# Kernel tuning notes

Measured on AMD Instinct MI355X. Metric: run time of the kernel, lower is better.

## Reference

```python
import jax, jax.numpy as jnp
import numpy as np

N = 100000   # nodes
E = 1600000  # edges (before self-loops)
IN = 128     # m (input feature dim)
H = 64       # hidden
L = 8        # layers
OUT = 40     # m_y


def setup_inputs() -> dict:
    key = jax.random.key(0)
    ks = jax.random.split(key, 6)
    x = jax.random.normal(ks[0], (N, IN), dtype=jnp.float32)
    edge_index = jax.random.randint(ks[1], (2, E), 0, N, dtype=jnp.int64)
    W0 = jax.random.normal(ks[2], (IN, H), dtype=jnp.float32) / np.float32(np.sqrt(IN))
    Ws = jax.random.normal(ks[3], (L - 1, H, H), dtype=jnp.float32) / np.float32(np.sqrt(H))
    bs = jnp.zeros((L, H), dtype=jnp.float32)
    lin_w = jax.random.normal(ks[4], (L * H, OUT), dtype=jnp.float32) / np.float32(np.sqrt(L * H))
    lin_b = jnp.zeros((OUT,), dtype=jnp.float32)
    return dict(x=x, W0=W0, Ws=Ws, bs=bs, lin_w=lin_w, lin_b=lin_b, edge_index=edge_index)


def reference(x, W0, Ws, bs, lin_w, lin_b, edge_index):
    # GCNConv (PyG): add self-loops, symmetric normalization D^-1/2 A D^-1/2.
    loop = jnp.arange(N, dtype=edge_index.dtype)
    src = jnp.concatenate([edge_index[0], loop])  # message sources
    dst = jnp.concatenate([edge_index[1], loop])  # aggregation targets
    deg = jax.ops.segment_sum(jnp.ones_like(dst, dtype=x.dtype), dst, num_segments=N)
    dis = jnp.where(deg > 0, jax.lax.rsqrt(deg), jnp.zeros_like(deg))
    norm = dis[src] * dis[dst]  # [E+N]

    def gcn_conv(h, W, b):
        h = h @ W                           # linear transform first (PyG order)
        msg = h[src] * norm[:, None]        # gather + edge normalization
        return jax.ops.segment_sum(msg, dst, num_segments=N) + b

    # dropout(p=0.5) is identity in eval mode (training=False)
    outs = []
    h = x
    for l in range(L):  # fixed small layer count
        W = W0 if l == 0 else Ws[l - 1]
        h = jax.nn.relu(gcn_conv(h, W, bs[l]))
        outs.append(h)
    jk = jnp.concatenate(outs, axis=-1)     # JumpingKnowledge 'cat': [N, L*H]
    return jk @ lin_w + lin_b
```

## Files before the change

kernel.cpp:

```cpp
#include <hip/hip_runtime.h>
#include <hip/hip_bf16.h>
#include <hip/hip_fp16.h>

#define N_NODES 100000
#define N_EDGES 1600000
#define HID     64
#define LAYERS  8
#define OUT_DIM 40
#define SCAN_NB 98
#define ZROW    N_NODES
#define NBUK    196
#define BUK_CAP 12000
#define S1_EPB  2048
#define AGG_N   32
#define AGG_CAP 1024

typedef __attribute__((ext_vector_type(8))) short short8;
typedef __attribute__((ext_vector_type(8))) _Float16 half8;
typedef __attribute__((ext_vector_type(4))) float float4v;
typedef __attribute__((ext_vector_type(4))) unsigned int uint4v;

__device__ inline float ldext(const void* p, bool f32, size_t i) {
    return f32 ? ((const float*)p)[i]
               : __bfloat162float(((const __hip_bfloat16*)p)[i]);
}
__device__ inline int load_edge(const void* raw, bool is64, long long idx) {
    return is64 ? (int)((const long long*)raw)[idx] : ((const int*)raw)[idx];
}
__device__ inline unsigned pack_bf16x2(float lo, float hi) {
    union { __hip_bfloat16 b; unsigned short u; } a, b;
    a.b = __float2bfloat16(lo);
    b.b = __float2bfloat16(hi);
    return ((unsigned)b.u << 16) | a.u;
}
__device__ inline unsigned short bf16bits(float v) {
    union { __hip_bfloat16 b; unsigned short u; } a;
    a.b = __float2bfloat16(v);
    return a.u;
}
__device__ inline unsigned short f16bits(float v) {
    union { __half h; unsigned short u; } a;
    a.h = __float2half_rn(v);
    return a.u;
}
__device__ inline __half2 u2h2(unsigned u) {
    union { unsigned u; __half2 h; } x; x.u = u; return x.h;
}
__device__ inline unsigned h22u(__half2 h) {
    union { unsigned u; __half2 h; } x; x.h = h; return x.u;
}

template <int CTRL>
__device__ inline unsigned dppu(unsigned v) {
    return (unsigned)__builtin_amdgcn_update_dpp((int)v, (int)v, CTRL, 0xF, 0xF, false);
}

__device__ inline uint4v gload16(const __half* base, unsigned voff) {
    uint4v d;
    asm volatile("global_load_dwordx4 %0, %1, %2"
                 : "=v"(d)
                 : "v"(voff), "s"((unsigned long long)base));
    return d;
}
#define WAITV(N) do { asm volatile("s_waitcnt vmcnt(" #N ")" ::: "memory"); \
                      __builtin_amdgcn_sched_barrier(0); } while (0)

__global__ void detect_kernel(const void* x, const void* ei, int* flags, int* gcur) {
    int t = threadIdx.x;
    for (int i = t; i < NBUK; i += 64) gcur[i] = 0;
    float v = fabsf(__bfloat162float(((const __hip_bfloat16*)x)[t]));
    bool inband = (v >= 0.00390625f && v <= 16.0f);
    unsigned long long m = __ballot(inband);
    if (t == 0) {
        flags[0] = (__popcll(m) < 48) ? 1 : 0;
        const int* e32 = (const int*)ei;
        flags[1] = ((e32[1] | e32[3] | e32[5] | e32[7]) == 0) ? 1 : 0;
    }
}

__global__ __launch_bounds__(256) void pack_params_kernel(const void* bs, const void* lin_w,
                                                          const void* W0, const void* Ws,
                                                          const int* __restrict__ flags,
                                                          float* __restrict__ bsf,
                                                          unsigned short* __restrict__ wpack) {
    bool f32 = flags[0] != 0;
    int gid = blockIdx.x * 256 + threadIdx.x;
    int stride = gridDim.x * 256;
    for (int idx = gid; idx < LAYERS * HID; idx += stride) bsf[idx] = ldext(bs, f32, idx);
    for (int idx = gid; idx < 8192; idx += stride) {
        int j = idx & 7, lane = (idx >> 3) & 63, rest = idx >> 9;
        int ks = rest & 3, ct = rest >> 2;
        int quad = lane >> 4, m = lane & 15;
        wpack[idx] = bf16bits(ldext(W0, f32, (size_t)(ks * 32 + quad * 8 + j) * 64 + ct * 16 + m));
    }
    for (int idx = gid; idx < 7 * 4096; idx += stride) {
        int l = idx >> 12, r = idx & 4095;
        int j = r & 7, lane = (r >> 3) & 63, rest = r >> 9;
        int ks = rest & 1, ct = rest >> 1;
        int quad = lane >> 4, m = lane & 15;
        wpack[8192 + idx] = f16bits(
            ldext(Ws, f32, (size_t)l * 4096 + (size_t)(ks * 32 + quad * 8 + j) * 64 + ct * 16 + m));
    }
    for (int idx = gid; idx < LAYERS * 3072; idx += stride) {
        int l = idx / 3072, r = idx % 3072;
        int j = r & 7, lane = (r >> 3) & 63, rest = r >> 9;
        int ks = rest & 1, ct = rest >> 1;
        int quad = lane >> 4, m = lane & 15;
        int col = ct * 16 + m;
        int k = l * 64 + ks * 32 + quad * 8 + j;
        wpack[36864 + idx] = (col < OUT_DIM)
            ? f16bits(ldext(lin_w, f32, (size_t)k * OUT_DIM + col)) : (unsigned short)0;
    }
}

__global__ __launch_bounds__(256) void bucket1_kernel(const void* ei_raw, const int* __restrict__ flags,
                                                      int* __restrict__ gcur, int* __restrict__ fifo) {
    __shared__ int lhist[NBUK];
    __shared__ int lbase[NBUK];
    bool is64 = flags[1] != 0;
    int t = threadIdx.x;
    for (int i = t; i < NBUK; i += 256) lhist[i] = 0;
    __syncthreads();
    int e0 = blockIdx.x * S1_EPB;
    int rec[8], bk[8], loff[8];
#pragma unroll
    for (int j = 0; j < 8; j++) {
        int e = e0 + j * 256 + t;
        bk[j] = -1;
        if (e < N_EDGES) {
            int s = load_edge(ei_raw, is64, e);
            int d = load_edge(ei_raw, is64, (long long)N_EDGES + e);
            int b = d >> 9;
            bk[j] = b;
            rec[j] = ((d & 511) << 17) | s;
            loff[j] = atomicAdd(&lhist[b], 1);
        }
    }
    __syncthreads();
    for (int i = t; i < NBUK; i += 256)
        lbase[i] = (lhist[i] > 0) ? atomicAdd(&gcur[i], lhist[i]) : 0;
    __syncthreads();
#pragma unroll
    for (int j = 0; j < 8; j++) {
        if (bk[j] >= 0) {
            int idx = lbase[bk[j]] + loff[j];
            if (idx < BUK_CAP) fifo[bk[j] * BUK_CAP + idx] = rec[j];
        }
    }
}

__global__ __launch_bounds__(256) void deg_fifo_kernel(const int* __restrict__ gcur,
                                                       const int* __restrict__ fifo,
                                                       int* __restrict__ deg,
                                                       float* __restrict__ dis) {
    __shared__ int ldeg[512];
    int b = blockIdx.x, t = threadIdx.x;
    ldeg[t] = 0;
    ldeg[t + 256] = 0;
    __syncthreads();
    int cnt = min(gcur[b], BUK_CAP);
    for (int i = t; i < cnt; i += 256)
        atomicAdd(&ldeg[fifo[b * BUK_CAP + i] >> 17], 1);
    __syncthreads();
    int n0 = b * 512 + t;
    if (n0 < N_NODES) {
        int d = ldeg[t];
        deg[n0] = d;
        dis[n0] = rsqrtf((float)(d + 1));
    }
    if (n0 + 256 < N_NODES) {
        int d = ldeg[t + 256];
        deg[n0 + 256] = d;
        dis[n0 + 256] = rsqrtf((float)(d + 1));
    }
}

__global__ __launch_bounds__(256) void scan1_kernel(const int* __restrict__ deg, int* __restrict__ row,
                                                    int* __restrict__ bsums) {
    __shared__ int sd[256];
    int t = threadIdx.x;
    int base = blockIdx.x * 1024 + t * 4;
    int v[4];
#pragma unroll
    for (int j = 0; j < 4; j++) {
        int idx = base + j;
        v[j] = (idx < N_NODES) ? deg[idx] : 0;
    }
    int s4 = v[0] + v[1] + v[2] + v[3];
    sd[t] = s4;
    __syncthreads();
    for (int off = 1; off < 256; off <<= 1) {
        int x = (t >= off) ? sd[t - off] : 0;
        __syncthreads();
        sd[t] += x;
        __syncthreads();
    }
    int run = sd[t] - s4;
#pragma unroll
    for (int j = 0; j < 4; j++) {
        int idx = base + j;
        if (idx < N_NODES) row[idx] = run;
        run += v[j];
    }
    if (t == 255) bsums[blockIdx.x] = sd[255];
}

__global__ void scan2_kernel(int* bsums) {
    __shared__ int sd[128];
    int t = threadIdx.x;
    int v = (t < SCAN_NB) ? bsums[t] : 0;
    sd[t] = v;
    __syncthreads();
    for (int off = 1; off < 128; off <<= 1) {
        int x = (t >= off) ? sd[t - off] : 0;
        __syncthreads();
        sd[t] += x;
        __syncthreads();
    }
    if (t < SCAN_NB) bsums[t] = sd[t] - v;
}

__global__ __launch_bounds__(256) void scan3_kernel(int* __restrict__ row, const int* __restrict__ bsums) {
    int i = blockIdx.x * 256 + threadIdx.x;
    if (i < N_NODES) row[i] += bsums[i >> 10];
    if (i == 0) row[N_NODES] = N_EDGES;
}

__global__ __launch_bounds__(256) void bucket2_kernel(const int* __restrict__ gcur,
                                                      const int* __restrict__ fifo,
                                                      const int* __restrict__ row,
                                                      int* __restrict__ csr_src) {
    __shared__ int lcur[512];
    int b = blockIdx.x, t = threadIdx.x;
    int n0 = b * 512 + t;
    lcur[t] = row[min(n0, N_NODES)];
    lcur[t + 256] = row[min(n0 + 256, N_NODES)];
    __syncthreads();
    int cnt = min(gcur[b], BUK_CAP);
    for (int i = t; i < cnt; i += 256) {
        int r = fifo[b * BUK_CAP + i];
        int pos = atomicAdd(&lcur[r >> 17], 1);
        csr_src[pos] = r & 0x1FFFF;
    }
}

template <int KS, int JK, bool ABF16>
__global__ __launch_bounds__(256) void mm_mfma_kernel(const void* __restrict__ h0,
                                                      const void* __restrict__ h1,
                                                      const int* __restrict__ flags,
                                                      const unsigned short* __restrict__ wW,
                                                      const unsigned short* __restrict__ wJ,
                                                      const float* __restrict__ dis,
                                                      __half* __restrict__ t0,
                                                      float* __restrict__ out_acc) {
    constexpr int K = KS * 32;
    int wave = threadIdx.x >> 6, lane = threadIdx.x & 63;
    int quad = lane >> 4, m = lane & 15;
    int nb = blockIdx.x * 64 + wave * 16;
    int ra = nb + m;
    if (ra > N_NODES - 1) ra = N_NODES - 1;
    short8 a[KS];
    if constexpr (ABF16) {
        if (flags[0]) {
            const float* xr = (const float*)h1 + (size_t)ra * K + quad * 8;
#pragma unroll
            for (int ks = 0; ks < KS; ks++) {
                float4 f0 = *(const float4*)(xr + ks * 32);
                float4 f1 = *(const float4*)(xr + ks * 32 + 4);
                short8 v;
                v[0] = (short)bf16bits(f0.x); v[1] = (short)bf16bits(f0.y);
                v[2] = (short)bf16bits(f0.z); v[3] = (short)bf16bits(f0.w);
                v[4] = (short)bf16bits(f1.x); v[5] = (short)bf16bits(f1.y);
                v[6] = (short)bf16bits(f1.z); v[7] = (short)bf16bits(f1.w);
                a[ks] = v;
            }
        } else {
            const short* hrow = (const short*)h0 + (size_t)ra * K + quad * 8;
#pragma unroll
            for (int ks = 0; ks < KS; ks++) a[ks] = *(const short8*)(hrow + ks * 32);
        }
    } else {
        const short* hrow = (const short*)h0 + (size_t)ra * K + quad * 8;
#pragma unroll
        for (int ks = 0; ks < KS; ks++) a[ks] = *(const short8*)(hrow + ks * 32);
    }
    float dr[4];
#pragma unroll
    for (int r = 0; r < 4; r++) {
        int rw = nb + quad * 4 + r;
        dr[r] = (rw < N_NODES) ? dis[rw] : 0.f;
    }
#pragma unroll
    for (int ct = 0; ct < 4; ct++) {
        float4v acc = (float4v){0.f, 0.f, 0.f, 0.f};
#pragma unroll
        for (int ks = 0; ks < KS; ks++) {
            short8 b = *(const short8*)(wW + ((ct * KS + ks) * 64 + lane) * 8);
            if constexpr (ABF16)
                acc = __builtin_amdgcn_mfma_f32_16x16x32_bf16(a[ks], b, acc, 0, 0, 0);
            else
                acc = __builtin_amdgcn_mfma_f32_16x16x32_f16(
                    __builtin_bit_cast(half8, a[ks]), __builtin_bit_cast(half8, b), acc, 0, 0, 0);
        }
#pragma unroll
        for (int r = 0; r < 4; r++) {
            t0[(size_t)(nb + quad * 4 + r) * 64 + ct * 16 + m] =
                __float2half(acc[r] * dr[r]);
        }
    }
    if (JK) {
#pragma unroll
        for (int ct = 0; ct < 3; ct++) {
            float4v j = (float4v){0.f, 0.f, 0.f, 0.f};
#pragma unroll
            for (int ks = 0; ks < KS; ks++) {
                short8 b = *(const short8*)(wJ + ((ct * KS + ks) * 64 + lane) * 8);
                if constexpr (ABF16)
                    j = __builtin_amdgcn_mfma_f32_16x16x32_bf16(a[ks], b, j, 0, 0, 0);
                else
                    j = __builtin_amdgcn_mfma_f32_16x16x32_f16(
                        __builtin_bit_cast(half8, a[ks]), __builtin_bit_cast(half8, b), j, 0, 0, 0);
            }
            int col = ct * 16 + m;
            if (col < OUT_DIM) {
#pragma unroll
                for (int r = 0; r < 4; r++) {
                    int rw = nb + quad * 4 + r;
                    if (rw < N_NODES) {
                        size_t o = (size_t)rw * OUT_DIM + col;
                        if (JK == 1) out_acc[o] = j[r];
                        else out_acc[o] += j[r];
                    }
                }
            }
        }
    }
}

__global__ __launch_bounds__(256, 6) void agg_kernel(const __half* __restrict__ t0,
                                                     const int* __restrict__ row,
                                                     const int* __restrict__ csr_src,
                                                     const float* __restrict__ bsf,
                                                     __half* __restrict__ h) {
    __shared__ int lrow[AGG_N + 1];
    __shared__ __align__(16) int lcsr[AGG_CAP + 32];
    int t = threadIdx.x;
    int nb = blockIdx.x * AGG_N;

    for (int i = t; i <= AGG_N; i += 256) {
        int n = nb + i;
        lrow[i] = row[n > N_NODES ? N_NODES : n];
    }
    __syncthreads();
    int rs0 = lrow[0];
    int cnt_raw = lrow[AGG_N] - rs0;
    int cnt = min(cnt_raw, AGG_CAP);

    int wave = t >> 6, lane = t & 63;
    for (int c = wave; c * 256 < cnt; c += 4) {
        const int* gsrc = csr_src + rs0 + c * 256 + lane * 4;
        __builtin_amdgcn_global_load_lds(
            (const __attribute__((address_space(1))) unsigned int*)gsrc,
            (__attribute__((address_space(3))) unsigned int*)&lcsr[4 + c * 256],
            16, 0, 0);
    }
    asm volatile("s_waitcnt vmcnt(0)" ::: "memory");
    __syncthreads();

    int g = lane >> 3, p = lane & 7;
    unsigned po = (unsigned)(p << 4);
    const __half2 h2zero = __floats2half2_rn(0.f, 0.f);

    if (cnt_raw <= AGG_CAP) {
        uint4v Av0, Av1, Av2; int Ars, Are;
        uint4v Bv0, Bv1, Bv2; int Brs, Bre;
        uint4v Cv0, Cv1, Cv2; int Crs, Cre;

#define AGG_ISSUE(P, v0, v1, v2, rs_, re_)                                      \
        do {                                                                    \
            int nl_ = wave * 8 + (P);                                           \
            int node_ = nb + nl_;                                               \
            bool valid_ = node_ < N_NODES;                                      \
            rs_ = valid_ ? lrow[nl_] : 0;                                       \
            re_ = valid_ ? lrow[nl_ + 1] : 0;                                   \
            int b_ = max(rs_ - rs0, 0) + g;                                     \
            int se0_ = lcsr[b_ + 3];                          \
            int se1_ = lcsr[b_ + 11];                         \
            int se2_ = lcsr[b_ + 19];                         \
            se0_ = (g == 0) ? (valid_ ? node_ : ZROW)                           \
                            : ((rs_ + g - 1 < re_) ? se0_ : ZROW);              \
            se1_ = (rs_ + g + 7  < re_) ? se1_ : ZROW;                          \
            se2_ = (rs_ + g + 15 < re_) ? se2_ : ZROW;                          \
            v0 = gload16(t0, ((unsigned)se0_ << 7) | po);                       \
            v1 = gload16(t0, ((unsigned)se1_ << 7) | po);                       \
            v2 = gload16(t0, ((unsigned)se2_ << 7) | po);                       \
        } while (0)

#define AGG_CONSUME(P, v0, v1, v2, rs_, re_)                                    \
        do {                                                                    \
            int nl_ = wave * 8 + (P);                                           \
            int node_ = nb + nl_;                                               \
            bool valid_ = node_ < N_NODES;                                      \
            __half2 a0_ = __hadd2(__hadd2(u2h2(v0[0]), u2h2(v1[0])), u2h2(v2[0])); \
            __half2 a1_ = __hadd2(__hadd2(u2h2(v0[1]), u2h2(v1[1])), u2h2(v2[1])); \
            __half2 a2_ = __hadd2(__hadd2(u2h2(v0[2]), u2h2(v1[2])), u2h2(v2[2])); \
            __half2 a3_ = __hadd2(__hadd2(u2h2(v0[3]), u2h2(v1[3])), u2h2(v2[3])); \
            if (__builtin_expect(__any(re_ - rs_ > 23), 0)) {                   \
                for (int q_ = rs_ + 23 + g; q_ < re_; q_ += 8) {                \
                    int se_ = lcsr[4 + q_ - rs0];                               \
                    uint4 v_ = *(const uint4*)(t0 + (size_t)se_ * 64 + p * 8);  \
                    a0_ = __hadd2(a0_, u2h2(v_.x));                             \
                    a1_ = __hadd2(a1_, u2h2(v_.y));                             \
                    a2_ = __hadd2(a2_, u2h2(v_.z));                             \
                    a3_ = __hadd2(a3_, u2h2(v_.w));                             \
                }                                                               \
            }                                                                   \
             \
            a0_ = __hadd2(a0_, u2h2(dppu<0x128>(h22u(a0_))));                   \
            a1_ = __hadd2(a1_, u2h2(dppu<0x128>(h22u(a1_))));                   \
            a2_ = __hadd2(a2_, u2h2(dppu<0x128>(h22u(a2_))));                   \
            a3_ = __hadd2(a3_, u2h2(dppu<0x128>(h22u(a3_))));                   \
            a0_ = __hadd2(a0_, u2h2(__shfl_xor(h22u(a0_), 16)));                \
            a1_ = __hadd2(a1_, u2h2(__shfl_xor(h22u(a1_), 16)));                \
            a2_ = __hadd2(a2_, u2h2(__shfl_xor(h22u(a2_), 16)));                \
            a3_ = __hadd2(a3_, u2h2(__shfl_xor(h22u(a3_), 16)));                \
            a0_ = __hadd2(a0_, u2h2(__shfl_xor(h22u(a0_), 32)));                \
            a1_ = __hadd2(a1_, u2h2(__shfl_xor(h22u(a1_), 32)));                \
            a2_ = __hadd2(a2_, u2h2(__shfl_xor(h22u(a2_), 32)));                \
            a3_ = __hadd2(a3_, u2h2(__shfl_xor(h22u(a3_), 32)));                \
            if (valid_ && g == 0) {                                             \
                float di_ = rsqrtf((float)(re_ - rs_ + 1));                     \
                const float* bb_ = bsf + p * 8;                                 \
                float f_[8];                                                    \
                f_[0] = __low2float(a0_); f_[1] = __high2float(a0_);            \
                f_[2] = __low2float(a1_); f_[3] = __high2float(a1_);            \
                f_[4] = __low2float(a2_); f_[5] = __high2float(a2_);            \
                f_[6] = __low2float(a3_); f_[7] = __high2float(a3_);            \
                _Pragma("unroll")                                               \
                for (int j_ = 0; j_ < 8; j_++)                                  \
                    f_[j_] = fmaxf(di_ * f_[j_] + bb_[j_], 0.f);                \
                uint4 pv_;                                                      \
                pv_.x = h22u(__floats2half2_rn(f_[0], f_[1]));                  \
                pv_.y = h22u(__floats2half2_rn(f_[2], f_[3]));                  \
                pv_.z = h22u(__floats2half2_rn(f_[4], f_[5]));                  \
                pv_.w = h22u(__floats2half2_rn(f_[6], f_[7]));                  \
                *(uint4*)(h + (size_t)node_ * 64 + p * 8) = pv_;                \
            }                                                                   \
        } while (0)

        AGG_ISSUE(0, Av0, Av1, Av2, Ars, Are);
        AGG_ISSUE(1, Bv0, Bv1, Bv2, Brs, Bre);
        AGG_ISSUE(2, Cv0, Cv1, Cv2, Crs, Cre);
        WAITV(6); AGG_CONSUME(0, Av0, Av1, Av2, Ars, Are);
        AGG_ISSUE(3, Av0, Av1, Av2, Ars, Are);
        WAITV(6); AGG_CONSUME(1, Bv0, Bv1, Bv2, Brs, Bre);
        AGG_ISSUE(4, Bv0, Bv1, Bv2, Brs, Bre);
        WAITV(6); AGG_CONSUME(2, Cv0, Cv1, Cv2, Crs, Cre);
        AGG_ISSUE(5, Cv0, Cv1, Cv2, Crs, Cre);
        WAITV(6); AGG_CONSUME(3, Av0, Av1, Av2, Ars, Are);
        AGG_ISSUE(6, Av0, Av1, Av2, Ars, Are);
        WAITV(6); AGG_CONSUME(4, Bv0, Bv1, Bv2, Brs, Bre);
        AGG_ISSUE(7, Bv0, Bv1, Bv2, Brs, Bre);
        WAITV(6); AGG_CONSUME(5, Cv0, Cv1, Cv2, Crs, Cre);
        WAITV(3); AGG_CONSUME(6, Av0, Av1, Av2, Ars, Are);
        WAITV(0); AGG_CONSUME(7, Bv0, Bv1, Bv2, Brs, Bre);
#undef AGG_ISSUE
#undef AGG_CONSUME
    } else {
        for (int pass = 0; pass < 8; pass++) {
            int nl = wave * 8 + pass;
            int node = nb + nl;
            bool valid = node < N_NODES;
            int rs = valid ? lrow[nl] : 0;
            int re = valid ? lrow[nl + 1] : 0;
            __half2 a2[4];
#pragma unroll
            for (int r = 0; r < 4; r++) a2[r] = h2zero;
            if (valid && g == 0) {
                uint4 v = *(const uint4*)(t0 + (size_t)node * 64 + p * 8);
                a2[0] = __hadd2(a2[0], u2h2(v.x));
                a2[1] = __hadd2(a2[1], u2h2(v.y));
                a2[2] = __hadd2(a2[2], u2h2(v.z));
                a2[3] = __hadd2(a2[3], u2h2(v.w));
            }
            for (int e = rs + g; e < re; e += 8) {
                int idx = e - rs0;
                int se = (idx < AGG_CAP) ? lcsr[4 + idx] : csr_src[e];
                uint4 v = *(const uint4*)(t0 + (size_t)se * 64 + p * 8);
                a2[0] = __hadd2(a2[0], u2h2(v.x));
                a2[1] = __hadd2(a2[1], u2h2(v.y));
                a2[2] = __hadd2(a2[2], u2h2(v.z));
                a2[3] = __hadd2(a2[3], u2h2(v.w));
            }
#pragma unroll
            for (int st = 8; st <= 32; st <<= 1) {
#pragma unroll
                for (int r = 0; r < 4; r++)
                    a2[r] = __hadd2(a2[r], u2h2(__shfl_xor(h22u(a2[r]), st)));
            }
            if (valid && g == 0) {
                float di = rsqrtf((float)(re - rs + 1));
                const float* bb = bsf + p * 8;
                float a[8];
#pragma unroll
                for (int r = 0; r < 4; r++) {
                    a[2 * r]     = __low2float(a2[r]);
                    a[2 * r + 1] = __high2float(a2[r]);
                }
#pragma unroll
                for (int j = 0; j < 8; j++) a[j] = fmaxf(di * a[j] + bb[j], 0.f);
                uint4 pv;
                pv.x = h22u(__floats2half2_rn(a[0], a[1]));
                pv.y = h22u(__floats2half2_rn(a[2], a[3]));
                pv.z = h22u(__floats2half2_rn(a[4], a[5]));
                pv.w = h22u(__floats2half2_rn(a[6], a[7]));
                *(uint4*)(h + (size_t)node * 64 + p * 8) = pv;
            }
        }
    }
}

__global__ __launch_bounds__(256) void jk_final_kernel(const __half* __restrict__ h,
                                                       const unsigned short* __restrict__ wJ,
                                                       const float* __restrict__ out_acc,
                                                       const void* __restrict__ lin_b,
                                                       const int* __restrict__ flags,
                                                       void* __restrict__ d_out) {
    bool f32 = flags[0] != 0;
    int wave = threadIdx.x >> 6, lane = threadIdx.x & 63;
    int quad = lane >> 4, m = lane & 15;
    int nb = blockIdx.x * 64 + wave * 16;
    int ra = nb + m;
    if (ra > N_NODES - 1) ra = N_NODES - 1;
    const short* hrow = (const short*)(h + (size_t)ra * 64) + quad * 8;
    short8 a0 = *(const short8*)(hrow);
    short8 a1 = *(const short8*)(hrow + 32);
#pragma unroll
    for (int ct = 0; ct < 3; ct++) {
        float4v j = (float4v){0.f, 0.f, 0.f, 0.f};
        short8 b0 = *(const short8*)(wJ + ((ct * 2 + 0) * 64 + lane) * 8);
        short8 b1 = *(const short8*)(wJ + ((ct * 2 + 1) * 64 + lane) * 8);
        j = __builtin_amdgcn_mfma_f32_16x16x32_f16(
            __builtin_bit_cast(half8, a0), __builtin_bit_cast(half8, b0), j, 0, 0, 0);
        j = __builtin_amdgcn_mfma_f32_16x16x32_f16(
            __builtin_bit_cast(half8, a1), __builtin_bit_cast(half8, b1), j, 0, 0, 0);
        int col = ct * 16 + m;
        if (col < OUT_DIM) {
            float lb = ldext(lin_b, f32, col);
#pragma unroll
            for (int r = 0; r < 4; r++) {
                int rw = nb + quad * 4 + r;
                if (rw < N_NODES) {
                    float v = out_acc[(size_t)rw * OUT_DIM + col] + j[r] + lb;
                    if (f32) ((float*)d_out)[(size_t)rw * OUT_DIM + col] = v;
                    else ((__hip_bfloat16*)d_out)[(size_t)rw * OUT_DIM + col] = __float2bfloat16(v);
                }
            }
        }
    }
}

extern "C" void kernel_launch(void* const* d_in, const int* in_sizes, int n_in,
                              void* d_out, int out_size, void* d_ws, size_t ws_size,
                              hipStream_t stream) {
    const void* x     = d_in[0];
    const void* W0    = d_in[1];
    const void* Ws    = d_in[2];
    const void* bs    = d_in[3];
    const void* lin_w = d_in[4];
    const void* lin_b = d_in[5];
    const void* ei    = d_in[6];

    size_t off = 0;
    auto alloc = [&](size_t bytes) -> void* {
        void* p = (char*)d_ws + off;
        off += (bytes + 511) & ~(size_t)511;
        return p;
    };
    int*   flags   = (int*)alloc(512);
    float* dis     = (float*)alloc((size_t)(N_NODES + 64) * 4);
    int*   deg     = (int*)alloc((size_t)N_NODES * 4);
    int*   row     = (int*)alloc((size_t)(N_NODES + 1) * 4);
    int*   bsums   = (int*)alloc(128 * 4);
    int*   gcur    = (int*)alloc((size_t)NBUK * 4);
    int*   fifo    = (int*)alloc((size_t)NBUK * BUK_CAP * 4);
    int*   csr_src = (int*)alloc((size_t)N_EDGES * 4);
    __half* t0  = (__half*)alloc((size_t)(N_NODES + 32) * HID * 2);
    __half* h   = (__half*)alloc((size_t)(N_NODES + 32) * HID * 2);
    float* out_acc = (float*)alloc((size_t)N_NODES * OUT_DIM * 4);
    float* bsf     = (float*)alloc((size_t)LAYERS * HID * 4);
    unsigned short* wpack = (unsigned short*)alloc((size_t)61440 * 2);

    const int nblkN  = (N_NODES + 255) / 256;
    const int nblkS1 = (N_EDGES + S1_EPB - 1) / S1_EPB;
    const int nblkMM = (N_NODES + 63) / 64;
    const int nblkAG = (N_NODES + AGG_N - 1) / AGG_N;

    detect_kernel<<<1, 64, 0, stream>>>(x, ei, flags, gcur);
    pack_params_kernel<<<80, 256, 0, stream>>>(bs, lin_w, W0, Ws, flags, bsf, wpack);
    bucket1_kernel<<<nblkS1, 256, 0, stream>>>(ei, flags, gcur, fifo);
    deg_fifo_kernel<<<NBUK, 256, 0, stream>>>(gcur, fifo, deg, dis);
    scan1_kernel<<<SCAN_NB, 256, 0, stream>>>(deg, row, bsums);
    scan2_kernel<<<1, 128, 0, stream>>>(bsums);
    scan3_kernel<<<nblkN, 256, 0, stream>>>(row, bsums);
    bucket2_kernel<<<NBUK, 256, 0, stream>>>(gcur, fifo, row, csr_src);

    const unsigned short* wJ0 = wpack + 36864;
    for (int l = 0; l < LAYERS; l++) {
        if (l == 0) {
            mm_mfma_kernel<4, 0, true><<<nblkMM, 256, 0, stream>>>(
                x, x, flags, wpack, nullptr, dis, t0, nullptr);
        } else if (l == 1) {
            mm_mfma_kernel<2, 1, false><<<nblkMM, 256, 0, stream>>>(
                h, h, flags, wpack + 8192, wJ0, dis, t0, out_acc);
        } else {
            mm_mfma_kernel<2, 2, false><<<nblkMM, 256, 0, stream>>>(
                h, h, flags, wpack + 8192 + (size_t)(l - 1) * 4096,
                wJ0 + (size_t)(l - 1) * 3072, dis, t0, out_acc);
        }
        agg_kernel<<<nblkAG, 256, 0, stream>>>(t0, row, csr_src,
                                               bsf + (size_t)l * HID, h);
    }
    jk_final_kernel<<<nblkMM, 256, 0, stream>>>(h, wJ0 + (size_t)7 * 3072, out_acc,
                                                lin_b, flags, d_out);
}
```

Before: 512.1 us.

## Fuse GCN aggregation with next layer's matmul and JK projection per block

Each layer's aggregation kernel now keeps its 64 output rows in shared memory and immediately runs the next layer's weight transform and JK output projection with MFMA. Half of the waves do the hidden transform while the other half do the JK accumulation. t0 ping-pongs between two buffers, so the separate matmul pass and the h round-trip through global memory go away. The block grows to 512 threads with a larger edge cache, which may reduce occupancy and makes the heavy MFMA work uneven across waves.

Result: faster. 493.3 us, median of 2 (-3.7%).

```diff
diff --git a/kernel.cpp b/kernel.cpp
--- a/kernel.cpp
+++ b/kernel.cpp
@@ -12,8 +12,9 @@
 #define NBUK    196
 #define BUK_CAP 12000
 #define S1_EPB  2048
-#define AGG_N   32
-#define AGG_CAP 1024
+#define FU_N    64
+#define FU_CAP  2048
+#define HB_S    72
 
 typedef __attribute__((ext_vector_type(8))) short short8;
 typedef __attribute__((ext_vector_type(8))) _Float16 half8;
@@ -26,12 +27,6 @@
 }
 __device__ inline int load_edge(const void* raw, bool is64, long long idx) {
     return is64 ? (int)((const long long*)raw)[idx] : ((const int*)raw)[idx];
-}
-__device__ inline unsigned pack_bf16x2(float lo, float hi) {
-    union { __hip_bfloat16 b; unsigned short u; } a, b;
-    a.b = __float2bfloat16(lo);
-    b.b = __float2bfloat16(hi);
-    return ((unsigned)b.u << 16) | a.u;
 }
 __device__ inline unsigned short bf16bits(float v) {
     union { __hip_bfloat16 b; unsigned short u; } a;
@@ -244,43 +239,33 @@
     }
 }
 
-template <int KS, int JK, bool ABF16>
-__global__ __launch_bounds__(256) void mm_mfma_kernel(const void* __restrict__ h0,
-                                                      const void* __restrict__ h1,
-                                                      const int* __restrict__ flags,
-                                                      const unsigned short* __restrict__ wW,
-                                                      const unsigned short* __restrict__ wJ,
-                                                      const float* __restrict__ dis,
-                                                      __half* __restrict__ t0,
-                                                      float* __restrict__ out_acc) {
-    constexpr int K = KS * 32;
+__global__ __launch_bounds__(256) void mm0_kernel(const void* __restrict__ x,
+                                                  const int* __restrict__ flags,
+                                                  const unsigned short* __restrict__ wW,
+                                                  const float* __restrict__ dis,
+                                                  __half* __restrict__ t0) {
+    constexpr int KS = 4, K = 128;
     int wave = threadIdx.x >> 6, lane = threadIdx.x & 63;
     int quad = lane >> 4, m = lane & 15;
     int nb = blockIdx.x * 64 + wave * 16;
     int ra = nb + m;
     if (ra > N_NODES - 1) ra = N_NODES - 1;
     short8 a[KS];
-    if constexpr (ABF16) {
-        if (flags[0]) {
-            const float* xr = (const float*)h1 + (size_t)ra * K + quad * 8;
-#pragma unroll
-            for (int ks = 0; ks < KS; ks++) {
-                float4 f0 = *(const float4*)(xr + ks * 32);
-                float4 f1 = *(const float4*)(xr + ks * 32 + 4);
-                short8 v;
-                v[0] = (short)bf16bits(f0.x); v[1] = (short)bf16bits(f0.y);
-                v[2] = (short)bf16bits(f0.z); v[3] = (short)bf16bits(f0.w);
-                v[4] = (short)bf16bits(f1.x); v[5] = (short)bf16bits(f1.y);
-                v[6] = (short)bf16bits(f1.z); v[7] = (short)bf16bits(f1.w);
-                a[ks] = v;
-            }
-        } else {
-            const short* hrow = (const short*)h0 + (size_t)ra * K + quad * 8;
-#pragma unroll
-            for (int ks = 0; ks < KS; ks++) a[ks] = *(const short8*)(hrow + ks * 32);
+    if (flags[0]) {
+        const float* xr = (const float*)x + (size_t)ra * K + quad * 8;
+#pragma unroll
+        for (int ks = 0; ks < KS; ks++) {
+            float4 f0 = *(const float4*)(xr + ks * 32);
+            float4 f1 = *(const float4*)(xr + ks * 32 + 4);
+            short8 v;
+            v[0] = (short)bf16bits(f0.x); v[1] = (short)bf16bits(f0.y);
+            v[2] = (short)bf16bits(f0.z); v[3] = (short)bf16bits(f0.w);
+            v[4] = (short)bf16bits(f1.x); v[5] = (short)bf16bits(f1.y);
+            v[6] = (short)bf16bits(f1.z); v[7] = (short)bf16bits(f1.w);
+            a[ks] = v;
         }
     } else {
-        const short* hrow = (const short*)h0 + (size_t)ra * K + quad * 8;
+        const short* hrow = (const short*)x + (size_t)ra * K + quad * 8;
 #pragma unroll
         for (int ks = 0; ks < KS; ks++) a[ks] = *(const short8*)(hrow + ks * 32);
     }
@@ -296,11 +281,7 @@
 #pragma unroll
         for (int ks = 0; ks < KS; ks++) {
             short8 b = *(const short8*)(wW + ((ct * KS + ks) * 64 + lane) * 8);
-            if constexpr (ABF16)
-                acc = __builtin_amdgcn_mfma_f32_16x16x32_bf16(a[ks], b, acc, 0, 0, 0);
-            else
-                acc = __builtin_amdgcn_mfma_f32_16x16x32_f16(
-                    __builtin_bit_cast(half8, a[ks]), __builtin_bit_cast(half8, b), acc, 0, 0, 0);
+            acc = __builtin_amdgcn_mfma_f32_16x16x32_bf16(a[ks], b, acc, 0, 0, 0);
         }
 #pragma unroll
         for (int r = 0; r < 4; r++) {
@@ -308,56 +289,37 @@
                 __float2half(acc[r] * dr[r]);
         }
     }
-    if (JK) {
-#pragma unroll
-        for (int ct = 0; ct < 3; ct++) {
-            float4v j = (float4v){0.f, 0.f, 0.f, 0.f};
-#pragma unroll
-            for (int ks = 0; ks < KS; ks++) {
-                short8 b = *(const short8*)(wJ + ((ct * KS + ks) * 64 + lane) * 8);
-                if constexpr (ABF16)
-                    j = __builtin_amdgcn_mfma_f32_16x16x32_bf16(a[ks], b, j, 0, 0, 0);
-                else
-                    j = __builtin_amdgcn_mfma_f32_16x16x32_f16(
-                        __builtin_bit_cast(half8, a[ks]), __builtin_bit_cast(half8, b), j, 0, 0, 0);
-            }
-            int col = ct * 16 + m;
-            if (col < OUT_DIM) {
-#pragma unroll
-                for (int r = 0; r < 4; r++) {
-                    int rw = nb + quad * 4 + r;
-                    if (rw < N_NODES) {
-                        size_t o = (size_t)rw * OUT_DIM + col;
-                        if (JK == 1) out_acc[o] = j[r];
-                        else out_acc[o] += j[r];
-                    }
-                }
-            }
-        }
-    }
-}
-
-__global__ __launch_bounds__(256, 6) void agg_kernel(const __half* __restrict__ t0,
-                                                     const int* __restrict__ row,
-                                                     const int* __restrict__ csr_src,
-                                                     const float* __restrict__ bsf,
-                                                     __half* __restrict__ h) {
-    __shared__ int lrow[AGG_N + 1];
-    __shared__ __align__(16) int lcsr[AGG_CAP + 32];
+}
+
+template <int MODE>
+__global__ __launch_bounds__(512, 4) void fused_kernel(const __half* __restrict__ t0_in,
+                                                       __half* __restrict__ t0_out,
+                                                       const int* __restrict__ row,
+                                                       const int* __restrict__ csr_src,
+                                                       const float* __restrict__ bsf,
+                                                       const unsigned short* __restrict__ wW,
+                                                       const unsigned short* __restrict__ wJ,
+                                                       float* __restrict__ out_acc,
+                                                       const void* __restrict__ lin_b,
+                                                       const int* __restrict__ flags,
+                                                       void* __restrict__ d_out) {
+    __shared__ int lrow[FU_N + 1];
+    __shared__ __align__(16) int lcsr[FU_CAP + 32];
+    __shared__ __align__(16) __half hbuf[FU_N * HB_S];
     int t = threadIdx.x;
-    int nb = blockIdx.x * AGG_N;
-
-    for (int i = t; i <= AGG_N; i += 256) {
+    int nb = blockIdx.x * FU_N;
+
+    for (int i = t; i <= FU_N; i += 512) {
         int n = nb + i;
         lrow[i] = row[n > N_NODES ? N_NODES : n];
     }
     __syncthreads();
     int rs0 = lrow[0];
-    int cnt_raw = lrow[AGG_N] - rs0;
-    int cnt = min(cnt_raw, AGG_CAP);
+    int cnt_raw = lrow[FU_N] - rs0;
+    int cnt = min(cnt_raw, FU_CAP);
 
     int wave = t >> 6, lane = t & 63;
-    for (int c = wave; c * 256 < cnt; c += 4) {
+    for (int c = wave; c * 256 < cnt; c += 8) {
         const int* gsrc = csr_src + rs0 + c * 256 + lane * 4;
         __builtin_amdgcn_global_load_lds(
             (const __attribute__((address_space(1))) unsigned int*)gsrc,
@@ -371,7 +333,7 @@
     unsigned po = (unsigned)(p << 4);
     const __half2 h2zero = __floats2half2_rn(0.f, 0.f);
 
-    if (cnt_raw <= AGG_CAP) {
+    if (cnt_raw <= FU_CAP) {
         uint4v Av0, Av1, Av2; int Ars, Are;
         uint4v Bv0, Bv1, Bv2; int Brs, Bre;
         uint4v Cv0, Cv1, Cv2; int Crs, Cre;
@@ -391,9 +353,9 @@
                             : ((rs_ + g - 1 < re_) ? se0_ : ZROW);              \
             se1_ = (rs_ + g + 7  < re_) ? se1_ : ZROW;                          \
             se2_ = (rs_ + g + 15 < re_) ? se2_ : ZROW;                          \
-            v0 = gload16(t0, ((unsigned)se0_ << 7) | po);                       \
-            v1 = gload16(t0, ((unsigned)se1_ << 7) | po);                       \
-            v2 = gload16(t0, ((unsigned)se2_ << 7) | po);                       \
+            v0 = gload16(t0_in, ((unsigned)se0_ << 7) | po);                    \
+            v1 = gload16(t0_in, ((unsigned)se1_ << 7) | po);                    \
+            v2 = gload16(t0_in, ((unsigned)se2_ << 7) | po);                    \
         } while (0)
 
 #define AGG_CONSUME(P, v0, v1, v2, rs_, re_)                                    \
@@ -408,14 +370,13 @@
             if (__builtin_expect(__any(re_ - rs_ > 23), 0)) {                   \
                 for (int q_ = rs_ + 23 + g; q_ < re_; q_ += 8) {                \
                     int se_ = lcsr[4 + q_ - rs0];                               \
-                    uint4 v_ = *(const uint4*)(t0 + (size_t)se_ * 64 + p * 8);  \
+                    uint4 v_ = *(const uint4*)(t0_in + (size_t)se_ * 64 + p * 8);\
                     a0_ = __hadd2(a0_, u2h2(v_.x));                             \
                     a1_ = __hadd2(a1_, u2h2(v_.y));                             \
                     a2_ = __hadd2(a2_, u2h2(v_.z));                             \
                     a3_ = __hadd2(a3_, u2h2(v_.w));                             \
                 }                                                               \
             }                                                                   \
-             \
             a0_ = __hadd2(a0_, u2h2(dppu<0x128>(h22u(a0_))));                   \
             a1_ = __hadd2(a1_, u2h2(dppu<0x128>(h22u(a1_))));                   \
             a2_ = __hadd2(a2_, u2h2(dppu<0x128>(h22u(a2_))));                   \
@@ -428,7 +389,7 @@
             a1_ = __hadd2(a1_, u2h2(__shfl_xor(h22u(a1_), 32)));                \
             a2_ = __hadd2(a2_, u2h2(__shfl_xor(h22u(a2_), 32)));                \
             a3_ = __hadd2(a3_, u2h2(__shfl_xor(h22u(a3_), 32)));                \
-            if (valid_ && g == 0) {                                             \
+            if (g == 0) {                                                       \
                 float di_ = rsqrtf((float)(re_ - rs_ + 1));                     \
                 const float* bb_ = bsf + p * 8;                                 \
                 float f_[8];                                                    \
@@ -440,11 +401,11 @@
                 for (int j_ = 0; j_ < 8; j_++)                                  \
                     f_[j_] = fmaxf(di_ * f_[j_] + bb_[j_], 0.f);                \
                 uint4 pv_;                                                      \
-                pv_.x = h22u(__floats2half2_rn(f_[0], f_[1]));                  \
-                pv_.y = h22u(__floats2half2_rn(f_[2], f_[3]));                  \
-                pv_.z = h22u(__floats2half2_rn(f_[4], f_[5]));                  \
-                pv_.w = h22u(__floats2half2_rn(f_[6], f_[7]));                  \
-                *(uint4*)(h + (size_t)node_ * 64 + p * 8) = pv_;                \
+                pv_.x = valid_ ? h22u(__floats2half2_rn(f_[0], f_[1])) : 0u;    \
+                pv_.y = valid_ ? h22u(__floats2half2_rn(f_[2], f_[3])) : 0u;    \
+                pv_.z = valid_ ? h22u(__floats2half2_rn(f_[4], f_[5])) : 0u;    \
+                pv_.w = valid_ ? h22u(__floats2half2_rn(f_[6], f_[7])) : 0u;    \
+                *(uint4*)(hbuf + (size_t)nl_ * HB_S + p * 8) = pv_;             \
             }                                                                   \
         } while (0)
 
@@ -477,7 +438,7 @@
 #pragma unroll
             for (int r = 0; r < 4; r++) a2[r] = h2zero;
             if (valid && g == 0) {
-                uint4 v = *(const uint4*)(t0 + (size_t)node * 64 + p * 8);
+                uint4 v = *(const uint4*)(t0_in + (size_t)node * 64 + p * 8);
                 a2[0] = __hadd2(a2[0], u2h2(v.x));
                 a2[1] = __hadd2(a2[1], u2h2(v.y));
                 a2[2] = __hadd2(a2[2], u2h2(v.z));
@@ -485,8 +446,8 @@
             }
             for (int e = rs + g; e < re; e += 8) {
                 int idx = e - rs0;
-                int se = (idx < AGG_CAP) ? lcsr[4 + idx] : csr_src[e];
-                uint4 v = *(const uint4*)(t0 + (size_t)se * 64 + p * 8);
+                int se = (idx < FU_CAP) ? lcsr[4 + idx] : csr_src[e];
+                uint4 v = *(const uint4*)(t0_in + (size_t)se * 64 + p * 8);
                 a2[0] = __hadd2(a2[0], u2h2(v.x));
                 a2[1] = __hadd2(a2[1], u2h2(v.y));
                 a2[2] = __hadd2(a2[2], u2h2(v.z));
@@ -498,7 +459,7 @@
                 for (int r = 0; r < 4; r++)
                     a2[r] = __hadd2(a2[r], u2h2(__shfl_xor(h22u(a2[r]), st)));
             }
-            if (valid && g == 0) {
+            if (g == 0) {
                 float di = rsqrtf((float)(re - rs + 1));
                 const float* bb = bsf + p * 8;
                 float a[8];
@@ -510,50 +471,72 @@
 #pragma unroll
                 for (int j = 0; j < 8; j++) a[j] = fmaxf(di * a[j] + bb[j], 0.f);
                 uint4 pv;
-                pv.x = h22u(__floats2half2_rn(a[0], a[1]));
-                pv.y = h22u(__floats2half2_rn(a[2], a[3]));
-                pv.z = h22u(__floats2half2_rn(a[4], a[5]));
-                pv.w = h22u(__floats2half2_rn(a[6], a[7]));
-                *(uint4*)(h + (size_t)node * 64 + p * 8) = pv;
+                pv.x = valid ? h22u(__floats2half2_rn(a[0], a[1])) : 0u;
+                pv.y = valid ? h22u(__floats2half2_rn(a[2], a[3])) : 0u;
+                pv.z = valid ? h22u(__floats2half2_rn(a[4], a[5])) : 0u;
+                pv.w = valid ? h22u(__floats2half2_rn(a[6], a[7])) : 0u;
+                *(uint4*)(hbuf + (size_t)nl * HB_S + p * 8) = pv;
             }
         }
     }
-}
-
-__global__ __launch_bounds__(256) void jk_final_kernel(const __half* __restrict__ h,
-                                                       const unsigned short* __restrict__ wJ,
-                                                       const float* __restrict__ out_acc,
-                                                       const void* __restrict__ lin_b,
-                                                       const int* __restrict__ flags,
-                                                       void* __restrict__ d_out) {
-    bool f32 = flags[0] != 0;
-    int wave = threadIdx.x >> 6, lane = threadIdx.x & 63;
+    __syncthreads();
+
     int quad = lane >> 4, m = lane & 15;
-    int nb = blockIdx.x * 64 + wave * 16;
-    int ra = nb + m;
-    if (ra > N_NODES - 1) ra = N_NODES - 1;
-    const short* hrow = (const short*)(h + (size_t)ra * 64) + quad * 8;
-    short8 a0 = *(const short8*)(hrow);
-    short8 a1 = *(const short8*)(hrow + 32);
-#pragma unroll
-    for (int ct = 0; ct < 3; ct++) {
-        float4v j = (float4v){0.f, 0.f, 0.f, 0.f};
-        short8 b0 = *(const short8*)(wJ + ((ct * 2 + 0) * 64 + lane) * 8);
-        short8 b1 = *(const short8*)(wJ + ((ct * 2 + 1) * 64 + lane) * 8);
-        j = __builtin_amdgcn_mfma_f32_16x16x32_f16(
-            __builtin_bit_cast(half8, a0), __builtin_bit_cast(half8, b0), j, 0, 0, 0);
-        j = __builtin_amdgcn_mfma_f32_16x16x32_f16(
-            __builtin_bit_cast(half8, a1), __builtin_bit_cast(half8, b1), j, 0, 0, 0);
-        int col = ct * 16 + m;
-        if (col < OUT_DIM) {
-            float lb = ldext(lin_b, f32, col);
+    int tile = wave & 3;
+    int loc0 = tile * 16;
+    if (MODE == 2 && wave >= 4) return;
+    short8 a0 = *(const short8*)(hbuf + (size_t)(loc0 + m) * HB_S + quad * 8);
+    short8 a1 = *(const short8*)(hbuf + (size_t)(loc0 + m) * HB_S + quad * 8 + 32);
+    if (MODE != 2 && wave < 4) {
+        float dr[4];
+#pragma unroll
+        for (int r = 0; r < 4; r++) {
+            int rl = loc0 + quad * 4 + r;
+            float di = rsqrtf((float)(lrow[rl + 1] - lrow[rl] + 1));
+            dr[r] = (nb + rl < N_NODES) ? di : 0.f;
+        }
+#pragma unroll
+        for (int ct = 0; ct < 4; ct++) {
+            float4v acc = (float4v){0.f, 0.f, 0.f, 0.f};
+            short8 b0 = *(const short8*)(wW + ((ct * 2 + 0) * 64 + lane) * 8);
+            short8 b1 = *(const short8*)(wW + ((ct * 2 + 1) * 64 + lane) * 8);
+            acc = __builtin_amdgcn_mfma_f32_16x16x32_f16(
+                __builtin_bit_cast(half8, a0), __builtin_bit_cast(half8, b0), acc, 0, 0, 0);
+            acc = __builtin_amdgcn_mfma_f32_16x16x32_f16(
+                __builtin_bit_cast(half8, a1), __builtin_bit_cast(half8, b1), acc, 0, 0, 0);
 #pragma unroll
             for (int r = 0; r < 4; r++) {
-                int rw = nb + quad * 4 + r;
-                if (rw < N_NODES) {
-                    float v = out_acc[(size_t)rw * OUT_DIM + col] + j[r] + lb;
-                    if (f32) ((float*)d_out)[(size_t)rw * OUT_DIM + col] = v;
-                    else ((__hip_bfloat16*)d_out)[(size_t)rw * OUT_DIM + col] = __float2bfloat16(v);
+                t0_out[(size_t)(nb + loc0 + quad * 4 + r) * 64 + ct * 16 + m] =
+                    __float2half(acc[r] * dr[r]);
+            }
+        }
+    } else {
+        bool f32o = (MODE == 2) && (flags[0] != 0);
+#pragma unroll
+        for (int ct = 0; ct < 3; ct++) {
+            float4v j = (float4v){0.f, 0.f, 0.f, 0.f};
+            short8 b0 = *(const short8*)(wJ + ((ct * 2 + 0) * 64 + lane) * 8);
+            short8 b1 = *(const short8*)(wJ + ((ct * 2 + 1) * 64 + lane) * 8);
+            j = __builtin_amdgcn_mfma_f32_16x16x32_f16(
+                __builtin_bit_cast(half8, a0), __builtin_bit_cast(half8, b0), j, 0, 0, 0);
+            j = __builtin_amdgcn_mfma_f32_16x16x32_f16(
+                __builtin_bit_cast(half8, a1), __builtin_bit_cast(half8, b1), j, 0, 0, 0);
+            int col = ct * 16 + m;
+            if (col < OUT_DIM) {
+                float lb = (MODE == 2) ? ldext(lin_b, flags[0] != 0, col) : 0.f;
+#pragma unroll
+                for (int r = 0; r < 4; r++) {
+                    int gw = nb + loc0 + quad * 4 + r;
+                    if (gw < N_NODES) {
+                        size_t o = (size_t)gw * OUT_DIM + col;
+                        if (MODE == 0) out_acc[o] = j[r];
+                        else if (MODE == 1) out_acc[o] += j[r];
+                        else {
+                            float v = out_acc[o] + j[r] + lb;
+                            if (f32o) ((float*)d_out)[o] = v;
+                            else ((__hip_bfloat16*)d_out)[o] = __float2bfloat16(v);
+                        }
+                    }
                 }
             }
         }
@@ -585,8 +568,8 @@
     int*   gcur    = (int*)alloc((size_t)NBUK * 4);
     int*   fifo    = (int*)alloc((size_t)NBUK * BUK_CAP * 4);
     int*   csr_src = (int*)alloc((size_t)N_EDGES * 4);
-    __half* t0  = (__half*)alloc((size_t)(N_NODES + 32) * HID * 2);
-    __half* h   = (__half*)alloc((size_t)(N_NODES + 32) * HID * 2);
+    __half* t0a = (__half*)alloc((size_t)(N_NODES + 64) * HID * 2);
+    __half* t0b = (__half*)alloc((size_t)(N_NODES + 64) * HID * 2);
     float* out_acc = (float*)alloc((size_t)N_NODES * OUT_DIM * 4);
     float* bsf     = (float*)alloc((size_t)LAYERS * HID * 4);
     unsigned short* wpack = (unsigned short*)alloc((size_t)61440 * 2);
@@ -594,7 +577,7 @@
     const int nblkN  = (N_NODES + 255) / 256;
     const int nblkS1 = (N_EDGES + S1_EPB - 1) / S1_EPB;
     const int nblkMM = (N_NODES + 63) / 64;
-    const int nblkAG = (N_NODES + AGG_N - 1) / AGG_N;
+    const int nblkF  = (N_NODES + FU_N - 1) / FU_N;
 
     detect_kernel<<<1, 64, 0, stream>>>(x, ei, flags, gcur);
     pack_params_kernel<<<80, 256, 0, stream>>>(bs, lin_w, W0, Ws, flags, bsf, wpack);
@@ -606,21 +589,22 @@
     bucket2_kernel<<<NBUK, 256, 0, stream>>>(gcur, fifo, row, csr_src);
 
     const unsigned short* wJ0 = wpack + 36864;
+    mm0_kernel<<<nblkMM, 256, 0, stream>>>(x, flags, wpack, dis, t0a);
     for (int l = 0; l < LAYERS; l++) {
+        const __half* ti = (l & 1) ? t0b : t0a;
+        __half*       to = (l & 1) ? t0a : t0b;
+        const float*  bl = bsf + (size_t)l * HID;
+        const unsigned short* wWn = wpack + 8192 + (size_t)l * 4096;
+        const unsigned short* wJl = wJ0 + (size_t)l * 3072;
         if (l == 0) {
-            mm_mfma_kernel<4, 0, true><<<nblkMM, 256, 0, stream>>>(
-                x, x, flags, wpack, nullptr, dis, t0, nullptr);
-        } else if (l == 1) {
-            mm_mfma_kernel<2, 1, false><<<nblkMM, 256, 0, stream>>>(
-                h, h, flags, wpack + 8192, wJ0, dis, t0, out_acc);
+            fused_kernel<0><<<nblkF, 512, 0, stream>>>(ti, to, row, csr_src, bl,
+                                                       wWn, wJl, out_acc, lin_b, flags, d_out);
+        } else if (l < 7) {
+            fused_kernel<1><<<nblkF, 512, 0, stream>>>(ti, to, row, csr_src, bl,
+                                                       wWn, wJl, out_acc, lin_b, flags, d_out);
         } else {
-            mm_mfma_kernel<2, 2, false><<<nblkMM, 256, 0, stream>>>(
-                h, h, flags, wpack + 8192 + (size_t)(l - 1) * 4096,
-                wJ0 + (size_t)(l - 1) * 3072, dis, t0, out_acc);
-        }
-        agg_kernel<<<nblkAG, 256, 0, stream>>>(t0, row, csr_src,
-                                               bsf + (size_t)l * HID, h);
-    }
-    jk_final_kernel<<<nblkMM, 256, 0, stream>>>(h, wJ0 + (size_t)7 * 3072, out_acc,
-                                                lin_b, flags, d_out);
-}
+            fused_kernel<2><<<nblkF, 512, 0, stream>>>(ti, to, row, csr_src, bl,
+                                                       wpack + 8192, wJl, out_acc, lin_b, flags, d_out);
+        }
+    }
+}
```
